# Kernel tuning notes

Measured on AMD Instinct MI355X. Metric: run time of the kernel, lower is better.

Reference implementation:

```python
import jax, jax.numpy as jnp
import numpy as np

N_NODES = 100000
N_EDGES = 1600000
N_GRAPHS = 2048
DIM_IN, DIM_H, DIM_FC, DIM_OUT = 128, 128, 256, 8


def _glorot(key, shape):
    fan_in, fan_out = shape[0], shape[1]
    lim = float(np.sqrt(6.0 / (fan_in + fan_out)))
    return jax.random.uniform(key, shape, jnp.float32, -lim, lim)


def setup_inputs() -> dict:
    key = jax.random.key(0)
    ks = jax.random.split(key, 16)
    x = jax.random.normal(ks[0], (N_NODES, DIM_IN), jnp.float32)
    edge_index = jax.random.randint(ks[1], (2, N_EDGES), 0, N_NODES, jnp.int64)
    batch = jnp.sort(jax.random.randint(ks[2], (N_NODES,), 0, N_GRAPHS, jnp.int64))
    inp = {"x": x, "edge_index": edge_index, "batch": batch}
    # GraphConv layers: W_rel [in,out], W_root [in,out], b [out]
    dims = [(DIM_IN, DIM_H), (DIM_H, DIM_H), (DIM_H, DIM_H), (DIM_H, DIM_H)]
    for i, (di, do) in enumerate(dims, start=1):
        inp[f"W{i}_rel"] = _glorot(ks[2 + 3 * i], (di, do))
        inp[f"W{i}_root"] = _glorot(ks[3 + 3 * i], (di, do))
        inp[f"b{i}"] = jnp.zeros((do,), jnp.float32)
    inp["fc_w"] = _glorot(ks[3], (DIM_H, DIM_FC))
    inp["fc_b"] = jnp.zeros((DIM_FC,), jnp.float32)
    inp["reg_w"] = _glorot(ks[4], (DIM_FC, DIM_OUT))
    inp["reg_b"] = jnp.zeros((DIM_OUT,), jnp.float32)
    return inp


def _graph_conv(x, src, dst, w_rel, w_root, b):
    # PyG GraphConv (aggr='add'): out_i = W_rel @ sum_{j->i} x_j + W_root @ x_i + b
    agg = jax.ops.segment_sum(x[src], dst, num_segments=N_NODES)  # [N, d_in]
    return agg @ w_rel + x @ w_root + b


def reference(x, edge_index, batch,
              W1_rel, W1_root, b1, W2_rel, W2_root, b2,
              W3_rel, W3_root, b3, W4_rel, W4_root, b4,
              fc_w, fc_b, reg_w, reg_b):
    src, dst = edge_index[0], edge_index[1]
    h = jax.nn.relu(_graph_conv(x, src, dst, W1_rel, W1_root, b1))
    h = jax.nn.relu(_graph_conv(h, src, dst, W2_rel, W2_root, b2))
    h = jax.nn.relu(_graph_conv(h, src, dst, W3_rel, W3_root, b3))
    h = jax.nn.relu(_graph_conv(h, src, dst, W4_rel, W4_root, b4))
    # global_mean_pool over graphs
    sums = jax.ops.segment_sum(h, batch, num_segments=N_GRAPHS)  # [G, d]
    cnt = jax.ops.segment_sum(jnp.ones((h.shape[0],), h.dtype), batch,
                              num_segments=N_GRAPHS)
    pooled = sums / jnp.maximum(cnt, 1.0)[:, None]
    # dropout is identity at inference
    hfc = pooled @ fc_w + fc_b
    return hfc @ reg_w + reg_b  # [G, dim_out]
```

## Files before the change

kernel.cpp:

```cpp
#include <hip/hip_runtime.h>

#define N_NODES 100000
#define N_EDGES 1600000
#define N_GRAPHS 2048
#define DIM 128

#define NBUK 196
#define BUKSH 9
#define NCH 256
#define EPB 6250
#define NMAT (NBUK * NCH)

typedef short short8v __attribute__((ext_vector_type(8)));
typedef float float4v __attribute__((ext_vector_type(4)));

__device__ __forceinline__ unsigned short f2bf(float f) {
  union { float f; unsigned u; } x; x.f = f;
  unsigned r = x.u + 0x7fffu + ((x.u >> 16) & 1u);
  return (unsigned short)(r >> 16);
}
__device__ __forceinline__ float bfhi2f(unsigned bits) {
  union { unsigned u; float f; } x; x.u = bits; return x.f;
}
__device__ __forceinline__ void accum8(float* p, uint4 v) {
  p[0] += bfhi2f(v.x << 16); p[1] += bfhi2f(v.x & 0xffff0000u);
  p[2] += bfhi2f(v.y << 16); p[3] += bfhi2f(v.y & 0xffff0000u);
  p[4] += bfhi2f(v.z << 16); p[5] += bfhi2f(v.z & 0xffff0000u);
  p[6] += bfhi2f(v.w << 16); p[7] += bfhi2f(v.w & 0xffff0000u);
}

__global__ __launch_bounds__(256) void k_bcount(const int* __restrict__ dst, int* __restrict__ cntmat) {
  __shared__ int cnt[NBUK];
  int b = blockIdx.x, t = threadIdx.x;
  if (t < NBUK) cnt[t] = 0;
  __syncthreads();
  int e0 = b * EPB;
  for (int j = t; j < EPB; j += 256) atomicAdd(&cnt[dst[e0 + j] >> BUKSH], 1);
  __syncthreads();
  if (t < NBUK) cntmat[t * NCH + b] = cnt[t];
}

__global__ __launch_bounds__(256) void k_scan1g(const int* __restrict__ in, int n,
                                                int* __restrict__ tmp, int* __restrict__ bsum) {
  __shared__ int sh[256];
  int b = blockIdx.x, t = threadIdx.x;
  int base = b * 1024 + t * 4;
  int v[4], s = 0;
#pragma unroll
  for (int i = 0; i < 4; i++) { v[i] = (base + i < n) ? in[base + i] : 0; s += v[i]; }
  sh[t] = s;
  __syncthreads();
  for (int off = 1; off < 256; off <<= 1) {
    int x = (t >= off) ? sh[t - off] : 0;
    __syncthreads();
    sh[t] += x;
    __syncthreads();
  }
  int run = sh[t] - s;
#pragma unroll
  for (int i = 0; i < 4; i++) { run += v[i]; if (base + i < n) tmp[base + i] = run; }
  if (t == 255) bsum[b] = sh[255];
}

__global__ void k_scan2g(int* __restrict__ bsum, int nb) {
  __shared__ int sh[128];
  int t = threadIdx.x;
  int v = (t < nb) ? bsum[t] : 0;
  sh[t] = v;
  __syncthreads();
  for (int off = 1; off < 128; off <<= 1) {
    int x = (t >= off) ? sh[t - off] : 0;
    __syncthreads();
    sh[t] += x;
    __syncthreads();
  }
  if (t < nb) bsum[t] = sh[t] - v;
}

__global__ __launch_bounds__(256) void k_exc(const int* __restrict__ tmp, const int* __restrict__ bsum,
                                             const int* __restrict__ in, int n, int* __restrict__ outExc) {
  int i = blockIdx.x * 256 + threadIdx.x;
  if (i < n) outExc[i] = tmp[i] + bsum[i >> 10] - in[i];
}

__global__ __launch_bounds__(256) void k_bscatter(const int* __restrict__ src, const int* __restrict__ dst,
                                                  const int* __restrict__ base, int2* __restrict__ epk) {
  __shared__ int cur[NBUK];
  int b = blockIdx.x, t = threadIdx.x;
  if (t < NBUK) cur[t] = base[t * NCH + b];
  __syncthreads();
  int e0 = b * EPB;
  for (int j = t; j < EPB; j += 256) {
    int s = src[e0 + j], d = dst[e0 + j];
    int pos = atomicAdd(&cur[d >> BUKSH], 1);
    epk[pos] = make_int2(s, d);
  }
}

__global__ __launch_bounds__(256) void k_bfinish(const int2* __restrict__ epk, const int* __restrict__ base,
                                                 int* __restrict__ rowptr, int* __restrict__ col) {
  __shared__ int a[512];
  __shared__ int sh[256];
  int k = blockIdx.x, t = threadIdx.x;
  int bstart = base[k * NCH];
  int bend = (k + 1 < NBUK) ? base[(k + 1) * NCH] : N_EDGES;
  a[t] = 0; a[t + 256] = 0;
  __syncthreads();
  for (int i = bstart + t; i < bend; i += 256) atomicAdd(&a[epk[i].y - (k << BUKSH)], 1);
  __syncthreads();
  int c0 = a[2 * t], c1 = a[2 * t + 1];
  int s = c0 + c1;
  sh[t] = s;
  __syncthreads();
  for (int off = 1; off < 256; off <<= 1) {
    int x = (t >= off) ? sh[t - off] : 0;
    __syncthreads();
    sh[t] += x;
    __syncthreads();
  }
  int excl = sh[t] - s;
  int st0 = bstart + excl;
  int st1 = st0 + c0;
  int g0 = (k << BUKSH) + 2 * t, g1 = g0 + 1;
  if (g0 < N_NODES) rowptr[g0] = st0;
  if (g1 < N_NODES) rowptr[g1] = st1;
  if (k == NBUK - 1 && t == 0) rowptr[N_NODES] = N_EDGES;
  __syncthreads();
  a[2 * t] = st0; a[2 * t + 1] = st1;
  __syncthreads();
  for (int i = bstart + t; i < bend; i += 256) {
    int2 e = epk[i];
    int pos = atomicAdd(&a[e.y - (k << BUKSH)], 1);
    col[pos] = e.x;
  }
}

__global__ __launch_bounds__(256) void k_gptr(const int* __restrict__ batch, int* __restrict__ gptr) {
  int i = blockIdx.x * 256 + threadIdx.x;
  if (i >= N_NODES) return;
  int b = batch[i];
  int a = (i == 0) ? -1 : batch[i - 1];
  for (int g = a + 1; g <= b; g++) gptr[g] = i;
  if (i == N_NODES - 1) {
    for (int g = b + 1; g <= N_GRAPHS; g++) gptr[g] = N_NODES;
  }
}

__global__ __launch_bounds__(256) void k_cvtx(const float* __restrict__ x, unsigned short* __restrict__ h) {
  int i = blockIdx.x * 256 + threadIdx.x;
  if (i < N_NODES * DIM / 4) {
    float4 v = ((const float4*)x)[i];
    unsigned lo = (unsigned)f2bf(v.x) | ((unsigned)f2bf(v.y) << 16);
    unsigned hi = (unsigned)f2bf(v.z) | ((unsigned)f2bf(v.w) << 16);
    ((uint2*)h)[i] = make_uint2(lo, hi);
  }
}

__global__ __launch_bounds__(256) void k_cvtw(const float* w0, const float* w1, const float* w2, const float* w3,
                                              const float* w4, const float* w5, const float* w6, const float* w7,
                                              unsigned short* __restrict__ wbF) {
  int i = blockIdx.x * 256 + threadIdx.x;
  if (i < 4 * 8 * 8 * 64 * 8) {
    int j = i & 7, l = (i >> 3) & 63, c = (i >> 9) & 7, kc = (i >> 12) & 7, layer = i >> 15;
    int m = layer * 2 + (kc >> 2);
    const float* w;
    switch (m) {
      case 0: w = w0; break; case 1: w = w1; break; case 2: w = w2; break; case 3: w = w3; break;
      case 4: w = w4; break; case 5: w = w5; break; case 6: w = w6; break; default: w = w7; break;
    }
    int kin = (kc & 3) * 32 + ((l >> 4) * 8) + j;
    int n = c * 16 + (l & 15);
    wbF[i] = f2bf(w[kin * 128 + n]);
  }
}

__global__ __launch_bounds__(64, 8) void k_fused(const int* __restrict__ rowptr,
                                                 const int* __restrict__ col,
                                                 const unsigned short* __restrict__ hIn,
                                                 const unsigned short* __restrict__ wbF,
                                                 const float* __restrict__ bias,
                                                 unsigned short* __restrict__ hOut) {
  __shared__ uint4 As[256];
  const int lane = threadIdx.x & 63;
  const int wrow0 = blockIdx.x * 16;
  const int sub = lane >> 4, li = lane & 15;

  for (int ri = 0; ri < 16; ri += 2) {
    int nodeA = wrow0 + ri;
    int nodeB = nodeA + 1;
    float pA[8], pB[8];
#pragma unroll
    for (int j = 0; j < 8; j++) { pA[j] = 0.f; pB[j] = 0.f; }
    int aS1 = 0, bS1 = 0, eA = 0, eB = 0;
    if (nodeA < N_NODES) { eA = rowptr[nodeA]; aS1 = rowptr[nodeA + 1]; }
    if (nodeB < N_NODES) { eB = rowptr[nodeB]; bS1 = rowptr[nodeB + 1]; }

    while (eA + 8 <= aS1 && eB + 8 <= bS1) {
      int cA0 = col[eA + sub], cA1 = col[eA + 4 + sub];
      int cB0 = col[eB + sub], cB1 = col[eB + 4 + sub];
      uint4 vA0 = *(const uint4*)(hIn + (size_t)cA0 * DIM + li * 8);
      uint4 vA1 = *(const uint4*)(hIn + (size_t)cA1 * DIM + li * 8);
      uint4 vB0 = *(const uint4*)(hIn + (size_t)cB0 * DIM + li * 8);
      uint4 vB1 = *(const uint4*)(hIn + (size_t)cB1 * DIM + li * 8);
      accum8(pA, vA0);
      accum8(pA, vA1);
      accum8(pB, vB0);
      accum8(pB, vB1);
      eA += 8; eB += 8;
    }
    for (; eA + 16 <= aS1; eA += 16) {
      int c0 = col[eA + sub], c1 = col[eA + 4 + sub], c2 = col[eA + 8 + sub], c3 = col[eA + 12 + sub];
      uint4 v0 = *(const uint4*)(hIn + (size_t)c0 * DIM + li * 8);
      uint4 v1 = *(const uint4*)(hIn + (size_t)c1 * DIM + li * 8);
      uint4 v2 = *(const uint4*)(hIn + (size_t)c2 * DIM + li * 8);
      uint4 v3 = *(const uint4*)(hIn + (size_t)c3 * DIM + li * 8);
      accum8(pA, v0); accum8(pA, v1); accum8(pA, v2); accum8(pA, v3);
    }
    if (eA + 8 <= aS1) {
      int c0 = col[eA + sub], c1 = col[eA + 4 + sub];
      uint4 v0 = *(const uint4*)(hIn + (size_t)c0 * DIM + li * 8);
      uint4 v1 = *(const uint4*)(hIn + (size_t)c1 * DIM + li * 8);
      accum8(pA, v0); accum8(pA, v1);
      eA += 8;
    }
    if (eA + 4 <= aS1) {
      int c0 = col[eA + sub];
      uint4 v0 = *(const uint4*)(hIn + (size_t)c0 * DIM + li * 8);
      accum8(pA, v0);
      eA += 4;
    }
    if (eA + sub < aS1) {
      int c0 = col[eA + sub];
      uint4 v0 = *(const uint4*)(hIn + (size_t)c0 * DIM + li * 8);
      accum8(pA, v0);
    }
    for (; eB + 16 <= bS1; eB += 16) {
      int c0 = col[eB + sub], c1 = col[eB + 4 + sub], c2 = col[eB + 8 + sub], c3 = col[eB + 12 + sub];
      uint4 v0 = *(const uint4*)(hIn + (size_t)c0 * DIM + li * 8);
      uint4 v1 = *(const uint4*)(hIn + (size_t)c1 * DIM + li * 8);
      uint4 v2 = *(const uint4*)(hIn + (size_t)c2 * DIM + li * 8);
      uint4 v3 = *(const uint4*)(hIn + (size_t)c3 * DIM + li * 8);
      accum8(pB, v0); accum8(pB, v1); accum8(pB, v2); accum8(pB, v3);
    }
    if (eB + 8 <= bS1) {
      int c0 = col[eB + sub], c1 = col[eB + 4 + sub];
      uint4 v0 = *(const uint4*)(hIn + (size_t)c0 * DIM + li * 8);
      uint4 v1 = *(const uint4*)(hIn + (size_t)c1 * DIM + li * 8);
      accum8(pB, v0); accum8(pB, v1);
      eB += 8;
    }
    if (eB + 4 <= bS1) {
      int c0 = col[eB + sub];
      uint4 v0 = *(const uint4*)(hIn + (size_t)c0 * DIM + li * 8);
      accum8(pB, v0);
      eB += 4;
    }
    if (eB + sub < bS1) {
      int c0 = col[eB + sub];
      uint4 v0 = *(const uint4*)(hIn + (size_t)c0 * DIM + li * 8);
      accum8(pB, v0);
    }

#pragma unroll
    for (int j = 0; j < 8; j++) {
      pA[j] += __shfl_xor(pA[j], 16, 64);
      pA[j] += __shfl_xor(pA[j], 32, 64);
      pB[j] += __shfl_xor(pB[j], 16, 64);
      pB[j] += __shfl_xor(pB[j], 32, 64);
    }
    if (sub == 0) {
      uint4 oA, oB;
      oA.x = (unsigned)f2bf(pA[0]) | ((unsigned)f2bf(pA[1]) << 16);
      oA.y = (unsigned)f2bf(pA[2]) | ((unsigned)f2bf(pA[3]) << 16);
      oA.z = (unsigned)f2bf(pA[4]) | ((unsigned)f2bf(pA[5]) << 16);
      oA.w = (unsigned)f2bf(pA[6]) | ((unsigned)f2bf(pA[7]) << 16);
      oB.x = (unsigned)f2bf(pB[0]) | ((unsigned)f2bf(pB[1]) << 16);
      oB.y = (unsigned)f2bf(pB[2]) | ((unsigned)f2bf(pB[3]) << 16);
      oB.z = (unsigned)f2bf(pB[4]) | ((unsigned)f2bf(pB[5]) << 16);
      oB.w = (unsigned)f2bf(pB[6]) | ((unsigned)f2bf(pB[7]) << 16);
      As[li * 16 + (ri ^ li)] = oA;
      As[li * 16 + ((ri + 1) ^ li)] = oB;
    }
  }

  float4v acc[8];
#pragma unroll
  for (int c2 = 0; c2 < 8; c2++)
#pragma unroll
    for (int i = 0; i < 4; i++) acc[c2][i] = 0.f;

#pragma unroll
  for (int kc = 0; kc < 4; kc++) {
    int c = kc * 4 + sub;
    short8v afr = *(const short8v*)&As[c * 16 + (li ^ c)];
#pragma unroll
    for (int c2 = 0; c2 < 8; c2++) {
      short8v bfr = *(const short8v*)(wbF + (size_t)((kc * 8 + c2) * 64 + lane) * 8);
      acc[c2] = __builtin_amdgcn_mfma_f32_16x16x32_bf16(afr, bfr, acc[c2], 0, 0, 0);
    }
  }

#pragma unroll
  for (int j = 0; j < 4; j++) {
    int idx = j * 64 + lane;
    int r = idx >> 4, c = idx & 15;
    int rsrc = wrow0 + r; if (rsrc > N_NODES - 1) rsrc = N_NODES - 1;
    uint4 v = *(const uint4*)(hIn + (size_t)rsrc * DIM + c * 8);
    As[c * 16 + (r ^ c)] = v;
  }

#pragma unroll
  for (int kc = 0; kc < 4; kc++) {
    int c = kc * 4 + sub;
    short8v afr = *(const short8v*)&As[c * 16 + (li ^ c)];
#pragma unroll
    for (int c2 = 0; c2 < 8; c2++) {
      short8v bfr = *(const short8v*)(wbF + (size_t)(((4 + kc) * 8 + c2) * 64 + lane) * 8);
      acc[c2] = __builtin_amdgcn_mfma_f32_16x16x32_bf16(afr, bfr, acc[c2], 0, 0, 0);
    }
  }

  int rbase = wrow0 + sub * 4;
#pragma unroll
  for (int c2 = 0; c2 < 8; c2++) {
    int colidx = c2 * 16 + li;
    float bv = bias[colidx];
#pragma unroll
    for (int i = 0; i < 4; i++) {
      int row = rbase + i;
      if (row < N_NODES) {
        float v = acc[c2][i] + bv;
        v = v > 0.f ? v : 0.f;
        hOut[row * DIM + colidx] = f2bf(v);
      }
    }
  }
}

__global__ __launch_bounds__(256) void k_pool(const unsigned short* __restrict__ h,
                                              const int* __restrict__ gptr,
                                              float* __restrict__ pooledMean) {
  int g = blockIdx.x * 4 + (threadIdx.x >> 6);
  if (g >= N_GRAPHS) return;
  int lane = threadIdx.x & 63;
  int li = lane & 15;
  int s0 = gptr[g], s1 = gptr[g + 1];
  float p[8];
#pragma unroll
  for (int j = 0; j < 8; j++) p[j] = 0.f;
  int f1 = s1 * 16;
  for (int f = s0 * 16 + lane; f < f1; f += 64) {
    uint4 v = ((const uint4*)h)[f];
    accum8(p, v);
  }
#pragma unroll
  for (int j = 0; j < 8; j++) {
    p[j] += __shfl_xor(p[j], 16, 64);
    p[j] += __shfl_xor(p[j], 32, 64);
  }
  float inv = (s1 > s0) ? 1.f / (float)(s1 - s0) : 0.f;
  if (lane < 16) {
    float4 o0 = make_float4(p[0] * inv, p[1] * inv, p[2] * inv, p[3] * inv);
    float4 o1 = make_float4(p[4] * inv, p[5] * inv, p[6] * inv, p[7] * inv);
    *(float4*)(pooledMean + g * DIM + li * 8) = o0;
    *(float4*)(pooledMean + g * DIM + li * 8 + 4) = o1;
  }
}

#define GPB 16
__global__ __launch_bounds__(256) void k_fc2(const float* __restrict__ pooledMean,
                                             const float* __restrict__ fc_w, const float* __restrict__ fc_b,
                                             const float* __restrict__ reg_w, const float* __restrict__ reg_b,
                                             float* __restrict__ out) {
  __shared__ float sp[GPB][128];
  __shared__ float shfc[GPB][257];
  int g0 = blockIdx.x * GPB, t = threadIdx.x;
  for (int k = t; k < GPB * 128; k += 256) sp[k >> 7][k & 127] = pooledMean[g0 * 128 + k];
  __syncthreads();
  float a[GPB];
  float fb = fc_b[t];
#pragma unroll
  for (int g = 0; g < GPB; g++) a[g] = fb;
  for (int k = 0; k < 128; k++) {
    float w = fc_w[k * 256 + t];
#pragma unroll
    for (int g = 0; g < GPB; g++) a[g] += sp[g][k] * w;
  }
#pragma unroll
  for (int g = 0; g < GPB; g++) shfc[g][t] = a[g];
  __syncthreads();
  if (t < GPB * 8) {
    int g = t >> 3, o = t & 7;
    float r = reg_b[o];
    for (int j = 0; j < 256; j++) r += shfc[g][j] * reg_w[j * 8 + o];
    out[(g0 + g) * 8 + o] = r;
  }
}

extern "C" void kernel_launch(void* const* d_in, const int* in_sizes, int n_in,
                              void* d_out, int out_size, void* d_ws, size_t ws_size,
                              hipStream_t stream) {
  (void)in_sizes; (void)n_in; (void)out_size; (void)ws_size;
  const float* x = (const float*)d_in[0];
  const int* ei = (const int*)d_in[1];
  const int* src = ei;
  const int* dst = ei + N_EDGES;
  const int* batch = (const int*)d_in[2];
  const float* Wrel[4]  = {(const float*)d_in[3], (const float*)d_in[6], (const float*)d_in[9],  (const float*)d_in[12]};
  const float* Wroot[4] = {(const float*)d_in[4], (const float*)d_in[7], (const float*)d_in[10], (const float*)d_in[13]};
  const float* bias[4]  = {(const float*)d_in[5], (const float*)d_in[8], (const float*)d_in[11], (const float*)d_in[14]};
  const float* fc_w  = (const float*)d_in[15];
  const float* fc_b  = (const float*)d_in[16];
  const float* reg_w = (const float*)d_in[17];
  const float* reg_b = (const float*)d_in[18];
  float* out = (float*)d_out;

  char* ws = (char*)d_ws;
  size_t off = 0;
  auto alloc = [&](size_t b) -> char* {
    char* p = ws + off;
    off = (off + b + 255) & ~(size_t)255;
    return p;
  };
  int* rowptr = (int*)alloc((N_NODES + 1) * 4);
  int* cntmat = (int*)alloc((size_t)NMAT * 4);
  int* tmpB   = (int*)alloc((size_t)NMAT * 4);
  int* bsumB  = (int*)alloc(128 * 4);
  int* base   = (int*)alloc((size_t)NMAT * 4);
  int2* epk   = (int2*)alloc((size_t)N_EDGES * 8);
  int* colws  = (int*)alloc((size_t)N_EDGES * 4);
  int* gptr   = (int*)alloc((N_GRAPHS + 1) * 4);
  unsigned short* wbF = (unsigned short*)alloc((size_t)4 * 32768 * 2);
  unsigned short* h_a = (unsigned short*)alloc((size_t)N_NODES * DIM * 2);
  unsigned short* h_b = (unsigned short*)alloc((size_t)N_NODES * DIM * 2);
  float* pooled = (float*)alloc((size_t)N_GRAPHS * DIM * 4);

  k_bcount<<<NCH, 256, 0, stream>>>(dst, cntmat);
  k_scan1g<<<NMAT / 1024, 256, 0, stream>>>(cntmat, NMAT, tmpB, bsumB);
  k_scan2g<<<1, 128, 0, stream>>>(bsumB, NMAT / 1024);
  k_exc<<<(NMAT + 255) / 256, 256, 0, stream>>>(tmpB, bsumB, cntmat, NMAT, base);
  k_bscatter<<<NCH, 256, 0, stream>>>(src, dst, base, epk);
  k_bfinish<<<NBUK, 256, 0, stream>>>(epk, base, rowptr, colws);

  k_gptr<<<(N_NODES + 255) / 256, 256, 0, stream>>>(batch, gptr);
  k_cvtx<<<(N_NODES * DIM / 4 + 255) / 256, 256, 0, stream>>>(x, h_a);
  k_cvtw<<<(4 * 32768 + 255) / 256, 256, 0, stream>>>(
      Wrel[0], Wroot[0], Wrel[1], Wroot[1], Wrel[2], Wroot[2], Wrel[3], Wroot[3], wbF);

  unsigned short* h_in = h_a;
  unsigned short* h_out = h_b;
  const int FB = N_NODES / 16;
  for (int l = 0; l < 4; l++) {
    k_fused<<<FB, 64, 0, stream>>>(rowptr, colws, h_in, wbF + (size_t)l * 32768, bias[l], h_out);
    unsigned short* t2 = h_in; h_in = h_out; h_out = t2;
  }

  k_pool<<<(N_GRAPHS + 3) / 4, 256, 0, stream>>>(h_in, gptr, pooled);
  k_fc2<<<N_GRAPHS / GPB, 256, 0, stream>>>(pooled, fc_w, fc_b, reg_w, reg_b, out);
}
```

Baseline: 507.8 us.

## Gather neighbor features as per-row int8 with scales instead of bf16

Adds an int8 copy of each node's features with a per-row absmax scale, produced by a new conversion kernel for the input and by the fused layer epilogue for each layer's output. The edge aggregation gathers 8-byte int8 chunks plus a scale instead of 16-byte bf16 chunks, roughly halving the random-gather traffic. The self (root) term still reads bf16. This adds quantization error to the aggregated sums, an extra scale load per edge, more epilogue work with LDS staging, lower occupancy bounds, and the removal of several bounds checks on node indices.

```diff
diff --git a/kernel.cpp b/kernel.cpp
--- a/kernel.cpp
+++ b/kernel.cpp
@@ -27,6 +27,15 @@
   p[2] += bfhi2f(v.y << 16); p[3] += bfhi2f(v.y & 0xffff0000u);
   p[4] += bfhi2f(v.z << 16); p[5] += bfhi2f(v.z & 0xffff0000u);
   p[6] += bfhi2f(v.w << 16); p[7] += bfhi2f(v.w & 0xffff0000u);
+}
+__device__ __forceinline__ float sb(unsigned w, int j) {
+  return (float)(int)(signed char)((w >> (8 * j)) & 0xffu);
+}
+__device__ __forceinline__ void accq(float* p, uint2 q, float s) {
+  p[0] += sb(q.x, 0) * s; p[1] += sb(q.x, 1) * s;
+  p[2] += sb(q.x, 2) * s; p[3] += sb(q.x, 3) * s;
+  p[4] += sb(q.y, 0) * s; p[5] += sb(q.y, 1) * s;
+  p[6] += sb(q.y, 2) * s; p[7] += sb(q.y, 3) * s;
 }
 
 __global__ __launch_bounds__(256) void k_bcount(const int* __restrict__ dst, int* __restrict__ cntmat) {
@@ -153,6 +162,26 @@
     unsigned lo = (unsigned)f2bf(v.x) | ((unsigned)f2bf(v.y) << 16);
     unsigned hi = (unsigned)f2bf(v.z) | ((unsigned)f2bf(v.w) << 16);
     ((uint2*)h)[i] = make_uint2(lo, hi);
+  }
+}
+
+__global__ __launch_bounds__(256) void k_cvtq(const float* __restrict__ x,
+                                              unsigned char* __restrict__ hq, float* __restrict__ sc) {
+  __shared__ char qb[4][128];
+  int wave = threadIdx.x >> 6, lane = threadIdx.x & 63;
+  int r = blockIdx.x * 4 + wave;
+  float a = x[(size_t)r * DIM + lane];
+  float b = x[(size_t)r * DIM + 64 + lane];
+  float m = fmaxf(fabsf(a), fabsf(b));
+#pragma unroll
+  for (int off = 1; off <= 32; off <<= 1) m = fmaxf(m, __shfl_xor(m, off, 64));
+  float inv = m > 0.f ? 127.f / m : 0.f;
+  if (lane == 0) sc[r] = m * (1.f / 127.f);
+  qb[wave][lane] = (char)(int)rintf(a * inv);
+  qb[wave][64 + lane] = (char)(int)rintf(b * inv);
+  if (lane < 8) {
+    uint4 v = *(const uint4*)&qb[wave][lane * 16];
+    *(uint4*)(hq + (size_t)r * DIM + lane * 16) = v;
   }
 }
 
@@ -174,12 +203,17 @@
   }
 }
 
-__global__ __launch_bounds__(64, 8) void k_fused(const int* __restrict__ rowptr,
+#define QLD(c) (*(const uint2*)(hq + (size_t)(c) * DIM + li * 8))
+__global__ __launch_bounds__(64, 6) void k_fused(const int* __restrict__ rowptr,
                                                  const int* __restrict__ col,
                                                  const unsigned short* __restrict__ hIn,
+                                                 const unsigned char* __restrict__ hq,
+                                                 const float* __restrict__ sc,
                                                  const unsigned short* __restrict__ wbF,
                                                  const float* __restrict__ bias,
-                                                 unsigned short* __restrict__ hOut) {
+                                                 unsigned short* __restrict__ hOut,
+                                                 unsigned char* __restrict__ hqOut,
+                                                 float* __restrict__ scOut) {
   __shared__ uint4 As[256];
   const int lane = threadIdx.x & 63;
   const int wrow0 = blockIdx.x * 16;
@@ -187,78 +221,73 @@
 
   for (int ri = 0; ri < 16; ri += 2) {
     int nodeA = wrow0 + ri;
-    int nodeB = nodeA + 1;
     float pA[8], pB[8];
 #pragma unroll
     for (int j = 0; j < 8; j++) { pA[j] = 0.f; pB[j] = 0.f; }
-    int aS1 = 0, bS1 = 0, eA = 0, eB = 0;
-    if (nodeA < N_NODES) { eA = rowptr[nodeA]; aS1 = rowptr[nodeA + 1]; }
-    if (nodeB < N_NODES) { eB = rowptr[nodeB]; bS1 = rowptr[nodeB + 1]; }
+    int eA = rowptr[nodeA], aS1 = rowptr[nodeA + 1];
+    int eB = aS1, bS1 = rowptr[nodeA + 2];
 
     while (eA + 8 <= aS1 && eB + 8 <= bS1) {
       int cA0 = col[eA + sub], cA1 = col[eA + 4 + sub];
       int cB0 = col[eB + sub], cB1 = col[eB + 4 + sub];
-      uint4 vA0 = *(const uint4*)(hIn + (size_t)cA0 * DIM + li * 8);
-      uint4 vA1 = *(const uint4*)(hIn + (size_t)cA1 * DIM + li * 8);
-      uint4 vB0 = *(const uint4*)(hIn + (size_t)cB0 * DIM + li * 8);
-      uint4 vB1 = *(const uint4*)(hIn + (size_t)cB1 * DIM + li * 8);
-      accum8(pA, vA0);
-      accum8(pA, vA1);
-      accum8(pB, vB0);
-      accum8(pB, vB1);
+      float sA0 = sc[cA0], sA1 = sc[cA1], sB0 = sc[cB0], sB1 = sc[cB1];
+      uint2 vA0 = QLD(cA0), vA1 = QLD(cA1);
+      uint2 vB0 = QLD(cB0), vB1 = QLD(cB1);
+      accq(pA, vA0, sA0); accq(pA, vA1, sA1);
+      accq(pB, vB0, sB0); accq(pB, vB1, sB1);
       eA += 8; eB += 8;
     }
     for (; eA + 16 <= aS1; eA += 16) {
       int c0 = col[eA + sub], c1 = col[eA + 4 + sub], c2 = col[eA + 8 + sub], c3 = col[eA + 12 + sub];
-      uint4 v0 = *(const uint4*)(hIn + (size_t)c0 * DIM + li * 8);
-      uint4 v1 = *(const uint4*)(hIn + (size_t)c1 * DIM + li * 8);
-      uint4 v2 = *(const uint4*)(hIn + (size_t)c2 * DIM + li * 8);
-      uint4 v3 = *(const uint4*)(hIn + (size_t)c3 * DIM + li * 8);
-      accum8(pA, v0); accum8(pA, v1); accum8(pA, v2); accum8(pA, v3);
+      float s0 = sc[c0], s1 = sc[c1], s2 = sc[c2], s3 = sc[c3];
+      uint2 v0 = QLD(c0), v1 = QLD(c1), v2 = QLD(c2), v3 = QLD(c3);
+      accq(pA, v0, s0); accq(pA, v1, s1); accq(pA, v2, s2); accq(pA, v3, s3);
     }
     if (eA + 8 <= aS1) {
       int c0 = col[eA + sub], c1 = col[eA + 4 + sub];
-      uint4 v0 = *(const uint4*)(hIn + (size_t)c0 * DIM + li * 8);
-      uint4 v1 = *(const uint4*)(hIn + (size_t)c1 * DIM + li * 8);
-      accum8(pA, v0); accum8(pA, v1);
+      float s0 = sc[c0], s1 = sc[c1];
+      uint2 v0 = QLD(c0), v1 = QLD(c1);
+      accq(pA, v0, s0); accq(pA, v1, s1);
       eA += 8;
     }
     if (eA + 4 <= aS1) {
       int c0 = col[eA + sub];
-      uint4 v0 = *(const uint4*)(hIn + (size_t)c0 * DIM + li * 8);
-      accum8(pA, v0);
+      float s0 = sc[c0];
+      uint2 v0 = QLD(c0);
+      accq(pA, v0, s0);
       eA += 4;
     }
     if (eA + sub < aS1) {
       int c0 = col[eA + sub];
-      uint4 v0 = *(const uint4*)(hIn + (size_t)c0 * DIM + li * 8);
-      accum8(pA, v0);
+      float s0 = sc[c0];
+      uint2 v0 = QLD(c0);
+      accq(pA, v0, s0);
     }
     for (; eB + 16 <= bS1; eB += 16) {
       int c0 = col[eB + sub], c1 = col[eB + 4 + sub], c2 = col[eB + 8 + sub], c3 = col[eB + 12 + sub];
-      uint4 v0 = *(const uint4*)(hIn + (size_t)c0 * DIM + li * 8);
-      uint4 v1 = *(const uint4*)(hIn + (size_t)c1 * DIM + li * 8);
-      uint4 v2 = *(const uint4*)(hIn + (size_t)c2 * DIM + li * 8);
-      uint4 v3 = *(const uint4*)(hIn + (size_t)c3 * DIM + li * 8);
-      accum8(pB, v0); accum8(pB, v1); accum8(pB, v2); accum8(pB, v3);
+      float s0 = sc[c0], s1 = sc[c1], s2 = sc[c2], s3 = sc[c3];
+      uint2 v0 = QLD(c0), v1 = QLD(c1), v2 = QLD(c2), v3 = QLD(c3);
+      accq(pB, v0, s0); accq(pB, v1, s1); accq(pB, v2, s2); accq(pB, v3, s3);
     }
     if (eB + 8 <= bS1) {
       int c0 = col[eB + sub], c1 = col[eB + 4 + sub];
-      uint4 v0 = *(const uint4*)(hIn + (size_t)c0 * DIM + li * 8);
-      uint4 v1 = *(const uint4*)(hIn + (size_t)c1 * DIM + li * 8);
-      accum8(pB, v0); accum8(pB, v1);
+      float s0 = sc[c0], s1 = sc[c1];
+      uint2 v0 = QLD(c0), v1 = QLD(c1);
+      accq(pB, v0, s0); accq(pB, v1, s1);
       eB += 8;
     }
     if (eB + 4 <= bS1) {
       int c0 = col[eB + sub];
-      uint4 v0 = *(const uint4*)(hIn + (size_t)c0 * DIM + li * 8);
-      accum8(pB, v0);
+      float s0 = sc[c0];
+      uint2 v0 = QLD(c0);
+      accq(pB, v0, s0);
       eB += 4;
     }
     if (eB + sub < bS1) {
       int c0 = col[eB + sub];
-      uint4 v0 = *(const uint4*)(hIn + (size_t)c0 * DIM + li * 8);
-      accum8(pB, v0);
+      float s0 = sc[c0];
+      uint2 v0 = QLD(c0);
+      accq(pB, v0, s0);
     }
 
 #pragma unroll
@@ -304,8 +333,7 @@
   for (int j = 0; j < 4; j++) {
     int idx = j * 64 + lane;
     int r = idx >> 4, c = idx & 15;
-    int rsrc = wrow0 + r; if (rsrc > N_NODES - 1) rsrc = N_NODES - 1;
-    uint4 v = *(const uint4*)(hIn + (size_t)rsrc * DIM + c * 8);
+    uint4 v = *(const uint4*)(hIn + (size_t)(wrow0 + r) * DIM + c * 8);
     As[c * 16 + (r ^ c)] = v;
   }
 
@@ -321,19 +349,57 @@
   }
 
   int rbase = wrow0 + sub * 4;
+  float bvv[8];
+  float m0 = 0.f, m1 = 0.f, m2 = 0.f, m3 = 0.f;
 #pragma unroll
   for (int c2 = 0; c2 < 8; c2++) {
     int colidx = c2 * 16 + li;
-    float bv = bias[colidx];
+    bvv[c2] = bias[colidx];
 #pragma unroll
     for (int i = 0; i < 4; i++) {
-      int row = rbase + i;
-      if (row < N_NODES) {
-        float v = acc[c2][i] + bv;
-        v = v > 0.f ? v : 0.f;
-        hOut[row * DIM + colidx] = f2bf(v);
-      }
-    }
+      float v = acc[c2][i] + bvv[c2];
+      v = v > 0.f ? v : 0.f;
+      hOut[(rbase + i) * DIM + colidx] = f2bf(v);
+      if (i == 0) m0 = fmaxf(m0, v);
+      else if (i == 1) m1 = fmaxf(m1, v);
+      else if (i == 2) m2 = fmaxf(m2, v);
+      else m3 = fmaxf(m3, v);
+    }
+  }
+#pragma unroll
+  for (int mask = 1; mask <= 8; mask <<= 1) {
+    m0 = fmaxf(m0, __shfl_xor(m0, mask, 64));
+    m1 = fmaxf(m1, __shfl_xor(m1, mask, 64));
+    m2 = fmaxf(m2, __shfl_xor(m2, mask, 64));
+    m3 = fmaxf(m3, __shfl_xor(m3, mask, 64));
+  }
+  float i0 = m0 > 0.f ? 127.f / m0 : 0.f;
+  float i1 = m1 > 0.f ? 127.f / m1 : 0.f;
+  float i2 = m2 > 0.f ? 127.f / m2 : 0.f;
+  float i3 = m3 > 0.f ? 127.f / m3 : 0.f;
+  if (li == 0) {
+    scOut[rbase + 0] = m0 * (1.f / 127.f);
+    scOut[rbase + 1] = m1 * (1.f / 127.f);
+    scOut[rbase + 2] = m2 * (1.f / 127.f);
+    scOut[rbase + 3] = m3 * (1.f / 127.f);
+  }
+  char* qb = (char*)As;
+#pragma unroll
+  for (int c2 = 0; c2 < 8; c2++) {
+#pragma unroll
+    for (int i = 0; i < 4; i++) {
+      float v = acc[c2][i] + bvv[c2];
+      v = v > 0.f ? v : 0.f;
+      float iv = (i == 0) ? i0 : (i == 1) ? i1 : (i == 2) ? i2 : i3;
+      qb[(sub * 4 + i) * 128 + c2 * 16 + li] = (char)(int)rintf(v * iv);
+    }
+  }
+  {
+    int k0 = lane, k1 = lane + 64;
+    uint4 w0 = *(const uint4*)(qb + k0 * 16);
+    uint4 w1 = *(const uint4*)(qb + k1 * 16);
+    *(uint4*)(hqOut + (size_t)(wrow0 + (k0 >> 3)) * DIM + (k0 & 7) * 16) = w0;
+    *(uint4*)(hqOut + (size_t)(wrow0 + (k1 >> 3)) * DIM + (k1 & 7) * 16) = w1;
   }
 }
 
@@ -433,6 +499,10 @@
   unsigned short* wbF = (unsigned short*)alloc((size_t)4 * 32768 * 2);
   unsigned short* h_a = (unsigned short*)alloc((size_t)N_NODES * DIM * 2);
   unsigned short* h_b = (unsigned short*)alloc((size_t)N_NODES * DIM * 2);
+  unsigned char* q_a  = (unsigned char*)alloc((size_t)N_NODES * DIM);
+  unsigned char* q_b  = (unsigned char*)alloc((size_t)N_NODES * DIM);
+  float* sc_a = (float*)alloc((size_t)N_NODES * 4);
+  float* sc_b = (float*)alloc((size_t)N_NODES * 4);
   float* pooled = (float*)alloc((size_t)N_GRAPHS * DIM * 4);
 
   k_bcount<<<NCH, 256, 0, stream>>>(dst, cntmat);
@@ -444,15 +514,20 @@
 
   k_gptr<<<(N_NODES + 255) / 256, 256, 0, stream>>>(batch, gptr);
   k_cvtx<<<(N_NODES * DIM / 4 + 255) / 256, 256, 0, stream>>>(x, h_a);
+  k_cvtq<<<N_NODES / 4, 256, 0, stream>>>(x, q_a, sc_a);
   k_cvtw<<<(4 * 32768 + 255) / 256, 256, 0, stream>>>(
       Wrel[0], Wroot[0], Wrel[1], Wroot[1], Wrel[2], Wroot[2], Wrel[3], Wroot[3], wbF);
 
-  unsigned short* h_in = h_a;
-  unsigned short* h_out = h_b;
+  unsigned short* h_in = h_a; unsigned short* h_out = h_b;
+  unsigned char* q_in = q_a;  unsigned char* q_out = q_b;
+  float* s_in = sc_a;         float* s_out = sc_b;
   const int FB = N_NODES / 16;
   for (int l = 0; l < 4; l++) {
-    k_fused<<<FB, 64, 0, stream>>>(rowptr, colws, h_in, wbF + (size_t)l * 32768, bias[l], h_out);
+    k_fused<<<FB, 64, 0, stream>>>(rowptr, colws, h_in, q_in, s_in,
+                                   wbF + (size_t)l * 32768, bias[l], h_out, q_out, s_out);
     unsigned short* t2 = h_in; h_in = h_out; h_out = t2;
+    unsigned char* t3 = q_in;  q_in = q_out;  q_out = t3;
+    float* t4 = s_in;          s_in = s_out;  s_out = t4;
   }
 
   k_pool<<<(N_GRAPHS + 3) / 4, 256, 0, stream>>>(h_in, gptr, pooled);
```

New measurement: 537.9 us. +5.9%, slower.
